# Performance work log

Measured on AMD Instinct MI355X. Metric: run time of the kernel, lower is better.

## Reference

```python
import jax, jax.numpy as jnp
import numpy as np

B, D, K, H, L = 8192, 512, 64, 256, 3  # batch, hidden width, rank_k, hypernet hidden, n layers


def _xavier(key, shape):
    fan_in, fan_out = shape[0], shape[1]
    std = float(np.sqrt(2.0 / (fan_in + fan_out)))
    return jax.random.normal(key, shape, dtype=jnp.float32) * std


def setup_inputs() -> dict:
    key = jax.random.key(0)
    ks = jax.random.split(key, 32)
    inp = {"x": jax.random.normal(ks[0], (B, D), dtype=jnp.float32)}
    i = 1
    for l in range(1, L + 1):
        inp[f"U{l}"] = _xavier(ks[i], (D, K)); i += 1
        inp[f"V{l}"] = _xavier(ks[i], (K, D)); i += 1
        # hypernet: cond_dim D -> H -> (K*K + D) [first D cols are bias]
        inp[f"hW1_{l}"] = _xavier(ks[i], (D, H)); i += 1
        inp[f"hb1_{l}"] = jnp.zeros((H,), dtype=jnp.float32)
        inp[f"hW2_{l}"] = _xavier(ks[i], (H, K * K + D)); i += 1
        inp[f"hb2_{l}"] = jnp.zeros((K * K + D,), dtype=jnp.float32)
    inp["Wout"] = _xavier(ks[i], (D, 1)); i += 1
    inp["bout"] = jnp.zeros((1,), dtype=jnp.float32)
    return inp


def _apg_layer(x, U, V, hW1, hb1, hW2, hb2):
    # hypernet (self-wise: condition_z = x)
    h1 = jax.nn.relu(x @ hW1 + hb1)            # [B, H]
    s = h1 @ hW2 + hb2                          # [B, K*K + D]
    bias = s[:, :D]                             # generated per-sample bias [B, D]
    S = s[:, D:].reshape(-1, K, K)              # per-sample weight [B, K, K]
    h = x @ U                                   # [B, K]
    h = jnp.einsum('bk,bkj->bj', h, S)          # bmm(h.unsqueeze(1), S).squeeze(1)
    out = h @ V + bias                          # [B, D]
    return jax.nn.relu(out)


def reference(x,
              U1, V1, hW1_1, hb1_1, hW2_1, hb2_1,
              U2, V2, hW1_2, hb1_2, hW2_2, hb2_2,
              U3, V3, hW1_3, hb1_3, hW2_3, hb2_3,
              Wout, bout):
    x = _apg_layer(x, U1, V1, hW1_1, hb1_1, hW2_1, hb2_1)
    x = _apg_layer(x, U2, V2, hW1_2, hb1_2, hW2_2, hb2_2)
    x = _apg_layer(x, U3, V3, hW1_3, hb1_3, hW2_3, hb2_3)
    return x @ Wout + bout                      # [B, 1]
```

## Files before the change

kernel.cpp:

```cpp
#include <hip/hip_runtime.h>

#define B_N 8192
#define D_N 512
#define K_N 64
#define H_N 256
#define SC  4608
#define R_T 32
#define NT  512

typedef __attribute__((ext_vector_type(8))) short short8;
typedef __attribute__((ext_vector_type(4))) short short4v;
typedef __attribute__((ext_vector_type(4))) float f32x4;

__device__ __forceinline__ unsigned short f2bf(float f) {
  unsigned int u = __builtin_bit_cast(unsigned int, f);
  u += 0x7fff + ((u >> 16) & 1);
  return (unsigned short)(u >> 16);
}
__device__ __forceinline__ float bf2f(unsigned short h) {
  unsigned int u = ((unsigned int)h) << 16;
  return __builtin_bit_cast(float, u);
}

#define L_ELEMS 1376256

struct PrepParams {
  const float* W1[3]; const float* U[3]; const float* W2[3]; const float* V[3];
  short* ws;
};

__global__ __launch_bounds__(256) void prep_weights(PrepParams p) {
  const int y = blockIdx.y;
  const int l = y / 5, m = y - 5 * l;
  short* wsl = p.ws + (size_t)l * L_ELEMS;
  if (m == 2) {
    const float* in = p.W2[l];
    short* out = wsl + 163840;
    const long total = 1048576;
    for (long e = (long)blockIdx.x * 256 + threadIdx.x; e < total;
         e += (long)gridDim.x * 256) {
      const int te = (int)(e & 7);
      const int j  = (int)((e >> 3) & 63);
      const int tc = (int)((e >> 9) & 31);
      const int kg = (int)(e >> 14);
      const int t  = tc * 8 + te;
      out[e] = (short)f2bf(in[(size_t)t * SC + 512 + 64 * kg + j]);
    }
    return;
  }
  const float* in; short* out; int K, istride, ioff, kshift;
  switch (m) {
    case 0: in = p.W1[l]; out = wsl;           K = 512; istride = 256;  ioff = 0; kshift = 9; break;
    case 1: in = p.U[l];  out = wsl + 131072;  K = 512; istride = 64;   ioff = 0; kshift = 9; break;
    case 3: in = p.W2[l]; out = wsl + 1212416; K = 256; istride = 4608; ioff = 0; kshift = 8; break;
    default:in = p.V[l];  out = wsl + 1343488; K = 64;  istride = 512;  ioff = 0; kshift = 6; break;
  }
  const long total = (long)K * ((m == 0) ? 256 : (m == 1) ? 64 : 512);
  for (long e = (long)blockIdx.x * 256 + threadIdx.x; e < total;
       e += (long)gridDim.x * 256) {
    const int k = (int)(e & (K - 1));
    const int n = (int)(e >> kshift);
    out[e] = (short)f2bf(in[(size_t)k * istride + ioff + n]);
  }
}

struct Params {
  const float* x;
  const float* b1[3];
  const float* b2[3];
  const float* Wout;
  const float* bout;
  const short* ws;
  float* out;
};

#define XP 520
#define HP 264
#define TP 72

__global__ __launch_bounds__(NT, 1) void apg_mfma(Params p) {
  __shared__ short xs[R_T][XP];
  __shared__ short h1s[R_T][HP];
  __shared__ short tmps[R_T][TP];
  __shared__ float hs[R_T][68];
  __shared__ float tpart[R_T][68];

  const int tid  = threadIdx.x;
  const int row0 = blockIdx.x * R_T;
  const int w    = tid >> 6;
  const int l15  = tid & 15;
  const int g    = (tid & 63) >> 4;
  const int koff = g * 8;
  const int rh   = w >> 2;
  const int nq   = w & 3;
  const int rbase = rh * 16;

  {
    const float4* xg = (const float4*)(p.x + (size_t)row0 * D_N);
    for (int i = tid; i < R_T * D_N / 4; i += NT) {
      float4 v = xg[i];
      const int r = i >> 7;
      const int c = (i & 127) << 2;
      short4v s4 = { (short)f2bf(v.x), (short)f2bf(v.y), (short)f2bf(v.z), (short)f2bf(v.w) };
      *(short4v*)&xs[r][c] = s4;
    }
  }
  __syncthreads();

  for (int l = 0; l < 3; ++l) {
    const short* wsl  = p.ws + (size_t)l * L_ELEMS;
    const short* W1T  = wsl;
    const short* UT   = wsl + 131072;
    const short* W2p  = wsl + 163840;
    const short* W2bT = wsl + 1212416;
    const short* VT   = wsl + 1343488;
    const float* b1 = p.b1[l];
    const float* b2 = p.b2[l];

    short8 aX[16];
#pragma unroll
    for (int kk = 0; kk < 16; ++kk)
      aX[kk] = *(const short8*)&xs[rbase + l15][kk * 32 + koff];

    for (int nf = 0; nf < 4; ++nf) {
      const int n0 = ((nq << 2) + nf) << 4;
      const short* pb = W1T + ((size_t)(n0 + l15) << 9) + koff;
      short8 bf[16];
#pragma unroll
      for (int kk = 0; kk < 16; ++kk) bf[kk] = *(const short8*)(pb + kk * 32);
      f32x4 acc = {0.f, 0.f, 0.f, 0.f};
#pragma unroll
      for (int kk = 0; kk < 16; ++kk)
        acc = __builtin_amdgcn_mfma_f32_16x16x32_bf16(aX[kk], bf[kk], acc, 0, 0, 0);
      const float bb = b1[n0 + l15];
#pragma unroll
      for (int i = 0; i < 4; ++i)
        h1s[rbase + g * 4 + i][n0 + l15] = (short)f2bf(fmaxf(acc[i] + bb, 0.f));
    }

    {
      const int n0 = nq << 4;
      const short* pb = UT + ((size_t)(n0 + l15) << 9) + koff;
      short8 bf[16];
#pragma unroll
      for (int kk = 0; kk < 16; ++kk) bf[kk] = *(const short8*)(pb + kk * 32);
      f32x4 acc = {0.f, 0.f, 0.f, 0.f};
#pragma unroll
      for (int kk = 0; kk < 16; ++kk)
        acc = __builtin_amdgcn_mfma_f32_16x16x32_bf16(aX[kk], bf[kk], acc, 0, 0, 0);
#pragma unroll
      for (int i = 0; i < 4; ++i) hs[rbase + g * 4 + i][n0 + l15] = acc[i];
    }
    __syncthreads();

    {
      const int kh  = w >> 2;
      const int kg0 = kh << 5;
      const int nl  = (nq << 4) + l15;
      short8 aH0[8], aH1[8];
#pragma unroll
      for (int kk = 0; kk < 8; ++kk) {
        aH0[kk] = *(const short8*)&h1s[l15][kk * 32 + koff];
        aH1[kk] = *(const short8*)&h1s[16 + l15][kk * 32 + koff];
      }
      float t0[4] = {0.f, 0.f, 0.f, 0.f}, t1[4] = {0.f, 0.f, 0.f, 0.f};
      {
        const float* pb2 = b2 + D_N + nl;
#pragma unroll 4
        for (int k = kg0; k < kg0 + 32; ++k) {
          const float b2v = pb2[k << 6];
#pragma unroll
          for (int i = 0; i < 4; ++i) {
            t0[i] += hs[g * 4 + i][k] * b2v;
            t1[i] += hs[16 + g * 4 + i][k] * b2v;
          }
        }
      }

      const short* gbase = W2p + (g << 9) + (nl << 3);
      short8 bA[8], bB[8];
      {
        const short* gp = gbase + ((size_t)kg0 << 14);
#pragma unroll
        for (int kk = 0; kk < 8; ++kk) bA[kk] = *(const short8*)(gp + (kk << 11));
      }
#pragma unroll 1
      for (int it = 0; it < 16; ++it) {
        const int kg = kg0 + it * 2;
        {
          const short* gp = gbase + ((size_t)(kg + 1) << 14);
#pragma unroll
          for (int kk = 0; kk < 8; ++kk) bB[kk] = *(const short8*)(gp + (kk << 11));
        }
        {
          f32x4 s0 = {0.f, 0.f, 0.f, 0.f}, s1 = {0.f, 0.f, 0.f, 0.f};
#pragma unroll
          for (int kk = 0; kk < 8; ++kk) {
            s0 = __builtin_amdgcn_mfma_f32_16x16x32_bf16(aH0[kk], bA[kk], s0, 0, 0, 0);
            s1 = __builtin_amdgcn_mfma_f32_16x16x32_bf16(aH1[kk], bA[kk], s1, 0, 0, 0);
          }
#pragma unroll
          for (int i = 0; i < 4; ++i) {
            t0[i] += hs[g * 4 + i][kg] * s0[i];
            t1[i] += hs[16 + g * 4 + i][kg] * s1[i];
          }
        }
        {
          const int kgn = (it == 15) ? (kg + 1) : (kg + 2);
          const short* gp = gbase + ((size_t)kgn << 14);
#pragma unroll
          for (int kk = 0; kk < 8; ++kk) bA[kk] = *(const short8*)(gp + (kk << 11));
        }
        {
          f32x4 s0 = {0.f, 0.f, 0.f, 0.f}, s1 = {0.f, 0.f, 0.f, 0.f};
#pragma unroll
          for (int kk = 0; kk < 8; ++kk) {
            s0 = __builtin_amdgcn_mfma_f32_16x16x32_bf16(aH0[kk], bB[kk], s0, 0, 0, 0);
            s1 = __builtin_amdgcn_mfma_f32_16x16x32_bf16(aH1[kk], bB[kk], s1, 0, 0, 0);
          }
#pragma unroll
          for (int i = 0; i < 4; ++i) {
            t0[i] += hs[g * 4 + i][kg + 1] * s0[i];
            t1[i] += hs[16 + g * 4 + i][kg + 1] * s1[i];
          }
        }
      }

      if (kh == 0) {
#pragma unroll
        for (int i = 0; i < 4; ++i) {
          tpart[g * 4 + i][nl]      = t0[i];
          tpart[16 + g * 4 + i][nl] = t1[i];
        }
      }
      __syncthreads();
      if (kh == 1) {
#pragma unroll
        for (int i = 0; i < 4; ++i) {
          tmps[g * 4 + i][nl]      = (short)f2bf(tpart[g * 4 + i][nl] + t0[i]);
          tmps[16 + g * 4 + i][nl] = (short)f2bf(tpart[16 + g * 4 + i][nl] + t1[i]);
        }
      }
    }
    __syncthreads();

    {
      short8 aT[2], aD[8];
#pragma unroll
      for (int kk = 0; kk < 2; ++kk)
        aT[kk] = *(const short8*)&tmps[rbase + l15][kk * 32 + koff];
#pragma unroll
      for (int kk = 0; kk < 8; ++kk)
        aD[kk] = *(const short8*)&h1s[rbase + l15][kk * 32 + koff];
      for (int ti = 0; ti < 8; ++ti) {
        const int n0 = ((ti << 2) + nq) << 4;
        const short* pv = VT + ((size_t)(n0 + l15) << 6) + koff;
        const short* pw = W2bT + ((size_t)(n0 + l15) << 8) + koff;
        short8 bv[2], bw[8];
#pragma unroll
        for (int kk = 0; kk < 2; ++kk) bv[kk] = *(const short8*)(pv + kk * 32);
#pragma unroll
        for (int kk = 0; kk < 8; ++kk) bw[kk] = *(const short8*)(pw + kk * 32);
        f32x4 acc = {0.f, 0.f, 0.f, 0.f};
#pragma unroll
        for (int kk = 0; kk < 2; ++kk)
          acc = __builtin_amdgcn_mfma_f32_16x16x32_bf16(aT[kk], bv[kk], acc, 0, 0, 0);
#pragma unroll
        for (int kk = 0; kk < 8; ++kk)
          acc = __builtin_amdgcn_mfma_f32_16x16x32_bf16(aD[kk], bw[kk], acc, 0, 0, 0);
        const float bb = b2[n0 + l15];
#pragma unroll
        for (int i = 0; i < 4; ++i)
          xs[rbase + g * 4 + i][n0 + l15] = (short)f2bf(fmaxf(acc[i] + bb, 0.f));
      }
    }
    __syncthreads();
  }

  {
    const int r  = tid >> 4;
    const int cl = tid & 15;
    float acc = 0.f;
    for (int c = cl; c < D_N; c += 16)
      acc = fmaf(bf2f((unsigned short)xs[r][c]), p.Wout[c], acc);
#pragma unroll
    for (int s = 1; s < 16; s <<= 1) acc += __shfl_xor(acc, s, 64);
    if (cl == 0) p.out[row0 + r] = acc + p.bout[0];
  }
}

extern "C" void kernel_launch(void* const* d_in, const int* in_sizes, int n_in,
                              void* d_out, int out_size, void* d_ws, size_t ws_size,
                              hipStream_t stream) {
  (void)in_sizes; (void)n_in; (void)ws_size; (void)out_size;
  PrepParams pp;
  Params p;
  p.x = (const float*)d_in[0];
  for (int l = 0; l < 3; ++l) {
    const int base = 1 + l * 6;
    pp.U[l]  = (const float*)d_in[base + 0];
    pp.V[l]  = (const float*)d_in[base + 1];
    pp.W1[l] = (const float*)d_in[base + 2];
    p.b1[l]  = (const float*)d_in[base + 3];
    pp.W2[l] = (const float*)d_in[base + 4];
    p.b2[l]  = (const float*)d_in[base + 5];
  }
  p.Wout = (const float*)d_in[19];
  p.bout = (const float*)d_in[20];
  p.ws   = (const short*)d_ws;
  p.out  = (float*)d_out;
  pp.ws  = (short*)d_ws;

  hipLaunchKernelGGL(prep_weights, dim3(1024, 15), dim3(256), 0, stream, pp);
  hipLaunchKernelGGL(apg_mfma, dim3(B_N / R_T), dim3(NT), 0, stream, p);
}
```

Baseline: 222.7 us.

## Double block to 1024 threads and split hypernet K-reduction four ways

Raises the block size from 512 to 1024 threads (16 waves) and redistributes work. Each wave now covers half as many W1, V and bias output tiles, and the S-contraction is split across four k-quarters instead of two. The partial sums go into a 4-deep tpart buffer and are reduced by a cooperative pass over all threads, which adds an extra barrier. The aim is more waves to hide the latency of weight loads from global memory. The cost is more shared memory, more per-wave A-fragment loads, and tighter register limits under launch_bounds(1024,4).

```diff
diff --git a/kernel.cpp b/kernel.cpp
--- a/kernel.cpp
+++ b/kernel.cpp
@@ -6,7 +6,7 @@
 #define H_N 256
 #define SC  4608
 #define R_T 32
-#define NT  512
+#define NT  1024
 
 typedef __attribute__((ext_vector_type(8))) short short8;
 typedef __attribute__((ext_vector_type(4))) short short4v;
@@ -78,12 +78,12 @@
 #define HP 264
 #define TP 72
 
-__global__ __launch_bounds__(NT, 1) void apg_mfma(Params p) {
+__global__ __launch_bounds__(NT, 4) void apg_mfma(Params p) {
   __shared__ short xs[R_T][XP];
   __shared__ short h1s[R_T][HP];
   __shared__ short tmps[R_T][TP];
   __shared__ float hs[R_T][68];
-  __shared__ float tpart[R_T][68];
+  __shared__ float tpart[4][R_T][68];
 
   const int tid  = threadIdx.x;
   const int row0 = blockIdx.x * R_T;
@@ -91,8 +91,8 @@
   const int l15  = tid & 15;
   const int g    = (tid & 63) >> 4;
   const int koff = g * 8;
-  const int rh   = w >> 2;
-  const int nq   = w & 3;
+  const int rh   = w >> 3;
+  const int wn   = w & 7;
   const int rbase = rh * 16;
 
   {
@@ -122,8 +122,8 @@
     for (int kk = 0; kk < 16; ++kk)
       aX[kk] = *(const short8*)&xs[rbase + l15][kk * 32 + koff];
 
-    for (int nf = 0; nf < 4; ++nf) {
-      const int n0 = ((nq << 2) + nf) << 4;
+    for (int nf = 0; nf < 2; ++nf) {
+      const int n0 = (wn << 5) + (nf << 4);
       const short* pb = W1T + ((size_t)(n0 + l15) << 9) + koff;
       short8 bf[16];
 #pragma unroll
@@ -138,8 +138,8 @@
         h1s[rbase + g * 4 + i][n0 + l15] = (short)f2bf(fmaxf(acc[i] + bb, 0.f));
     }
 
-    {
-      const int n0 = nq << 4;
+    if (wn < 4) {
+      const int n0 = wn << 4;
       const short* pb = UT + ((size_t)(n0 + l15) << 9) + koff;
       short8 bf[16];
 #pragma unroll
@@ -154,9 +154,10 @@
     __syncthreads();
 
     {
-      const int kh  = w >> 2;
-      const int kg0 = kh << 5;
-      const int nl  = (nq << 4) + l15;
+      const int nqc = w & 3;
+      const int kq  = (w >> 2) & 3;
+      const int kg0 = kq << 4;
+      const int nl  = (nqc << 4) + l15;
       short8 aH0[8], aH1[8];
 #pragma unroll
       for (int kk = 0; kk < 8; ++kk) {
@@ -167,7 +168,7 @@
       {
         const float* pb2 = b2 + D_N + nl;
 #pragma unroll 4
-        for (int k = kg0; k < kg0 + 32; ++k) {
+        for (int k = kg0; k < kg0 + 16; ++k) {
           const float b2v = pb2[k << 6];
 #pragma unroll
           for (int i = 0; i < 4; ++i) {
@@ -185,7 +186,7 @@
         for (int kk = 0; kk < 8; ++kk) bA[kk] = *(const short8*)(gp + (kk << 11));
       }
 #pragma unroll 1
-      for (int it = 0; it < 16; ++it) {
+      for (int it = 0; it < 8; ++it) {
         const int kg = kg0 + it * 2;
         {
           const short* gp = gbase + ((size_t)(kg + 1) << 14);
@@ -206,7 +207,7 @@
           }
         }
         {
-          const int kgn = (it == 15) ? (kg + 1) : (kg + 2);
+          const int kgn = (it == 7) ? (kg + 1) : (kg + 2);
           const short* gp = gbase + ((size_t)kgn << 14);
 #pragma unroll
           for (int kk = 0; kk < 8; ++kk) bA[kk] = *(const short8*)(gp + (kk << 11));
@@ -226,21 +227,19 @@
         }
       }
 
-      if (kh == 0) {
-#pragma unroll
-        for (int i = 0; i < 4; ++i) {
-          tpart[g * 4 + i][nl]      = t0[i];
-          tpart[16 + g * 4 + i][nl] = t1[i];
-        }
-      }
-      __syncthreads();
-      if (kh == 1) {
-#pragma unroll
-        for (int i = 0; i < 4; ++i) {
-          tmps[g * 4 + i][nl]      = (short)f2bf(tpart[g * 4 + i][nl] + t0[i]);
-          tmps[16 + g * 4 + i][nl] = (short)f2bf(tpart[16 + g * 4 + i][nl] + t1[i]);
-        }
-      }
+#pragma unroll
+      for (int i = 0; i < 4; ++i) {
+        tpart[kq][g * 4 + i][nl]      = t0[i];
+        tpart[kq][16 + g * 4 + i][nl] = t1[i];
+      }
+    }
+    __syncthreads();
+
+    for (int e = tid; e < R_T * K_N; e += NT) {
+      const int r = e >> 6;
+      const int c = e & 63;
+      const float s = ((tpart[0][r][c] + tpart[1][r][c]) + tpart[2][r][c]) + tpart[3][r][c];
+      tmps[r][c] = (short)f2bf(s);
     }
     __syncthreads();
 
@@ -252,8 +251,8 @@
 #pragma unroll
       for (int kk = 0; kk < 8; ++kk)
         aD[kk] = *(const short8*)&h1s[rbase + l15][kk * 32 + koff];
-      for (int ti = 0; ti < 8; ++ti) {
-        const int n0 = ((ti << 2) + nq) << 4;
+      for (int ti = 0; ti < 4; ++ti) {
+        const int n0 = ((ti << 3) + wn) << 4;
         const short* pv = VT + ((size_t)(n0 + l15) << 6) + koff;
         const short* pw = W2bT + ((size_t)(n0 + l15) << 8) + koff;
         short8 bv[2], bw[8];
@@ -277,7 +276,7 @@
     __syncthreads();
   }
 
-  {
+  if (tid < 512) {
     const int r  = tid >> 4;
     const int cl = tid & 15;
     float acc = 0.f;
```

Measured after the change: 228.4 us. 2.6% more time.

## Stream W2 tiles through per-wave LDS ring via global_load_lds triple buffering

Applied to the files above, without the earlier changes.

Replaces the register double-buffered global loads of the bf16 W2 weight tiles with a per-wave three-slot LDS ring filled by direct global-to-LDS loads, using manual vmcnt waits to keep about two chunks in flight. The prep kernel reorders W2 so that each 64-lane chunk is a contiguous 2048-element block matching the MFMA operand layout, and the ring aliases the xs buffer to save LDS. The aim is to hide global memory latency and cut VGPR pressure from holding sixteen short8 registers. The cost is tricky hand-written waitcnt ordering and a risk of hazards if xs is still live or if the counts are off.

```diff
diff --git a/kernel.cpp b/kernel.cpp
--- a/kernel.cpp
+++ b/kernel.cpp
@@ -39,12 +39,16 @@
     const long total = 1048576;
     for (long e = (long)blockIdx.x * 256 + threadIdx.x; e < total;
          e += (long)gridDim.x * 256) {
-      const int te = (int)(e & 7);
-      const int j  = (int)((e >> 3) & 63);
-      const int tc = (int)((e >> 9) & 31);
-      const int kg = (int)(e >> 14);
-      const int t  = tc * 8 + te;
-      out[e] = (short)f2bf(in[(size_t)t * SC + 512 + 64 * kg + j]);
+      const int te   = (int)(e & 7);
+      const int lane = (int)((e >> 3) & 63);
+      const int kk   = (int)((e >> 9) & 3);
+      const int nq   = (int)((e >> 11) & 3);
+      const int h2   = (int)((e >> 13) & 1);
+      const int kg   = (int)(e >> 14);
+      const int g    = lane >> 4;
+      const int l15  = lane & 15;
+      const int t    = h2 * 128 + kk * 32 + g * 8 + te;
+      out[e] = (short)f2bf(in[(size_t)t * SC + 512 + 64 * kg + nq * 16 + l15]);
     }
     return;
   }
@@ -78,16 +82,29 @@
 #define HP 264
 #define TP 72
 
+__device__ __forceinline__ void stage_chunk(const short* W2p, short* slotp,
+                                            int cglob, int nq, int lane) {
+  const short* gp = W2p + (((size_t)cglob * 4 + nq) << 11) + (lane << 3);
+#pragma unroll
+  for (int i = 0; i < 4; ++i) {
+    __builtin_amdgcn_global_load_lds(
+        (const __attribute__((address_space(1))) void*)(gp + (i << 9)),
+        (__attribute__((address_space(3))) void*)(slotp + (i << 9)), 16, 0, 0);
+  }
+}
+
 __global__ __launch_bounds__(NT, 1) void apg_mfma(Params p) {
-  __shared__ short xs[R_T][XP];
+  __shared__ __attribute__((aligned(16))) short ring[8][3][2048];
   __shared__ short h1s[R_T][HP];
   __shared__ short tmps[R_T][TP];
   __shared__ float hs[R_T][68];
   __shared__ float tpart[R_T][68];
+  short (*xs)[XP] = (short (*)[XP]) & ring[0][0][0];
 
   const int tid  = threadIdx.x;
   const int row0 = blockIdx.x * R_T;
   const int w    = tid >> 6;
+  const int lane = tid & 63;
   const int l15  = tid & 15;
   const int g    = (tid & 63) >> 4;
   const int koff = g * 8;
@@ -177,52 +194,58 @@
         }
       }
 
-      const short* gbase = W2p + (g << 9) + (nl << 3);
-      short8 bA[8], bB[8];
-      {
-        const short* gp = gbase + ((size_t)kg0 << 14);
-#pragma unroll
-        for (int kk = 0; kk < 8; ++kk) bA[kk] = *(const short8*)(gp + (kk << 11));
-      }
+      short* ringw = &ring[w][0][0];
+      const int cbase = kg0 << 1;
+
+      asm volatile("s_waitcnt vmcnt(0)" ::: "memory");
+      stage_chunk(W2p, ringw,        cbase + 0, nq, lane);
+      stage_chunk(W2p, ringw + 2048, cbase + 1, nq, lane);
+      stage_chunk(W2p, ringw + 4096, cbase + 2, nq, lane);
+
 #pragma unroll 1
-      for (int it = 0; it < 16; ++it) {
-        const int kg = kg0 + it * 2;
+      for (int kgi = 0; kgi < 32; ++kgi) {
+        const int kg = kg0 + kgi;
+        f32x4 s0 = {0.f, 0.f, 0.f, 0.f}, s1 = {0.f, 0.f, 0.f, 0.f};
         {
-          const short* gp = gbase + ((size_t)(kg + 1) << 14);
-#pragma unroll
-          for (int kk = 0; kk < 8; ++kk) bB[kk] = *(const short8*)(gp + (kk << 11));
+          const int slot = (2 * kgi) % 3;
+          if (kgi < 31) asm volatile("s_waitcnt vmcnt(8)" ::: "memory");
+          else          asm volatile("s_waitcnt vmcnt(4)" ::: "memory");
+          const short* rb = ringw + slot * 2048 + (lane << 3);
+          short8 bf[4];
+#pragma unroll
+          for (int kk = 0; kk < 4; ++kk) bf[kk] = *(const short8*)(rb + (kk << 9));
+          asm volatile("s_waitcnt lgkmcnt(0)" ::: "memory");
+          __builtin_amdgcn_sched_barrier(0);
+          if (kgi <= 30)
+            stage_chunk(W2p, ringw + slot * 2048, cbase + 2 * kgi + 3, nq, lane);
+#pragma unroll
+          for (int kk = 0; kk < 4; ++kk) {
+            s0 = __builtin_amdgcn_mfma_f32_16x16x32_bf16(aH0[kk], bf[kk], s0, 0, 0, 0);
+            s1 = __builtin_amdgcn_mfma_f32_16x16x32_bf16(aH1[kk], bf[kk], s1, 0, 0, 0);
+          }
         }
         {
-          f32x4 s0 = {0.f, 0.f, 0.f, 0.f}, s1 = {0.f, 0.f, 0.f, 0.f};
-#pragma unroll
-          for (int kk = 0; kk < 8; ++kk) {
-            s0 = __builtin_amdgcn_mfma_f32_16x16x32_bf16(aH0[kk], bA[kk], s0, 0, 0, 0);
-            s1 = __builtin_amdgcn_mfma_f32_16x16x32_bf16(aH1[kk], bA[kk], s1, 0, 0, 0);
+          const int slot = (2 * kgi + 1) % 3;
+          if (kgi < 31) asm volatile("s_waitcnt vmcnt(8)" ::: "memory");
+          else          asm volatile("s_waitcnt vmcnt(0)" ::: "memory");
+          const short* rb = ringw + slot * 2048 + (lane << 3);
+          short8 bf[4];
+#pragma unroll
+          for (int kk = 0; kk < 4; ++kk) bf[kk] = *(const short8*)(rb + (kk << 9));
+          asm volatile("s_waitcnt lgkmcnt(0)" ::: "memory");
+          __builtin_amdgcn_sched_barrier(0);
+          if (kgi <= 29)
+            stage_chunk(W2p, ringw + slot * 2048, cbase + 2 * kgi + 4, nq, lane);
+#pragma unroll
+          for (int kk = 0; kk < 4; ++kk) {
+            s0 = __builtin_amdgcn_mfma_f32_16x16x32_bf16(aH0[4 + kk], bf[kk], s0, 0, 0, 0);
+            s1 = __builtin_amdgcn_mfma_f32_16x16x32_bf16(aH1[4 + kk], bf[kk], s1, 0, 0, 0);
           }
-#pragma unroll
-          for (int i = 0; i < 4; ++i) {
-            t0[i] += hs[g * 4 + i][kg] * s0[i];
-            t1[i] += hs[16 + g * 4 + i][kg] * s1[i];
-          }
-        }
-        {
-          const int kgn = (it == 15) ? (kg + 1) : (kg + 2);
-          const short* gp = gbase + ((size_t)kgn << 14);
-#pragma unroll
-          for (int kk = 0; kk < 8; ++kk) bA[kk] = *(const short8*)(gp + (kk << 11));
-        }
-        {
-          f32x4 s0 = {0.f, 0.f, 0.f, 0.f}, s1 = {0.f, 0.f, 0.f, 0.f};
-#pragma unroll
-          for (int kk = 0; kk < 8; ++kk) {
-            s0 = __builtin_amdgcn_mfma_f32_16x16x32_bf16(aH0[kk], bB[kk], s0, 0, 0, 0);
-            s1 = __builtin_amdgcn_mfma_f32_16x16x32_bf16(aH1[kk], bB[kk], s1, 0, 0, 0);
-          }
-#pragma unroll
-          for (int i = 0; i < 4; ++i) {
-            t0[i] += hs[g * 4 + i][kg + 1] * s0[i];
-            t1[i] += hs[16 + g * 4 + i][kg + 1] * s1[i];
-          }
+        }
+#pragma unroll
+        for (int i = 0; i < 4; ++i) {
+          t0[i] += hs[g * 4 + i][kg] * s0[i];
+          t1[i] += hs[16 + g * 4 + i][kg] * s1[i];
         }
       }
 
```

Measured after the change: 216.3 us (median of 2 runs). 1.03x faster.
